# Kernel optimization log

Hardware: AMD Instinct MI355X
Metric: run time of the kernel (lower is better)

The kernel has to match this reference:

```python
import jax, jax.numpy as jnp
import numpy as np
from jax import lax

EMBED = 768
D_INNER = 2 * EMBED          # expand = 2
D_STATE = 16
D_CONV = 4
DT_RANK = (EMBED + 15) // 16  # 48
FF = 3072
B, L = 2, 1024


def setup_inputs() -> dict:
    key = jax.random.key(0)
    ks = jax.random.split(key, 20)
    s = 0.02
    inp = {
        "x": jax.random.normal(ks[0], (B, L, EMBED), jnp.float32),
        # Mamba params
        "in_proj_w": jax.random.normal(ks[1], (2 * D_INNER, EMBED), jnp.float32) * s,
        "conv_w": jax.random.normal(ks[2], (D_INNER, 1, D_CONV), jnp.float32) * s,
        "conv_b": jnp.zeros((D_INNER,), jnp.float32),
        "x_proj_w": jax.random.normal(ks[3], (DT_RANK + 2 * D_STATE, D_INNER), jnp.float32) * s,
        "dt_proj_w": jax.random.normal(ks[4], (D_INNER, DT_RANK), jnp.float32) * s,
        "dt_proj_b": jax.random.normal(ks[5], (D_INNER,), jnp.float32) * s,
        "A_log": jnp.log(jnp.broadcast_to(jnp.arange(1, D_STATE + 1, dtype=jnp.float32), (D_INNER, D_STATE))),
        "D_param": jnp.ones((D_INNER,), jnp.float32),
        "out_proj_w": jax.random.normal(ks[6], (EMBED, D_INNER), jnp.float32) * s,
        # block params
        "ln1_w": jnp.ones((EMBED,), jnp.float32), "ln1_b": jnp.zeros((EMBED,), jnp.float32),
        "ln2_w": jnp.ones((EMBED,), jnp.float32), "ln2_b": jnp.zeros((EMBED,), jnp.float32),
        "ffn_w1": jax.random.normal(ks[7], (FF, EMBED), jnp.float32) * s,
        "ffn_b1": jnp.zeros((FF,), jnp.float32),
        "ffn_w2": jax.random.normal(ks[8], (EMBED, FF), jnp.float32) * s,
        "ffn_b2": jnp.zeros((EMBED,), jnp.float32),
    }
    return inp


def _layernorm(x, w, b, eps=1e-5):
    mu = jnp.mean(x, -1, keepdims=True)
    var = jnp.mean((x - mu) ** 2, -1, keepdims=True)
    return (x - mu) * lax.rsqrt(var + eps) * w + b


def _mamba(x, in_proj_w, conv_w, conv_b, x_proj_w, dt_proj_w, dt_proj_b,
           A_log, D_param, out_proj_w):
    # x: [B, L, E]
    xz = jnp.einsum('ble,de->bld', x, in_proj_w)          # [B,L,2*Di]
    xin, z = jnp.split(xz, 2, axis=-1)                    # [B,L,Di] each
    # causal depthwise conv over time
    xc = lax.conv_general_dilated(
        xin.transpose(0, 2, 1), conv_w, window_strides=(1,),
        padding=[(D_CONV - 1, 0)], feature_group_count=D_INNER,
        dimension_numbers=('NCH', 'OIH', 'NCH'))
    xc = (xc + conv_b[None, :, None]).transpose(0, 2, 1)  # [B,L,Di]
    xc = jax.nn.silu(xc)
    # input-dependent SSM params
    x_dbl = jnp.einsum('bld,rd->blr', xc, x_proj_w)       # [B,L,dt_rank+2n]
    dt, Bm, Cm = jnp.split(x_dbl, [DT_RANK, DT_RANK + D_STATE], axis=-1)
    delta = jax.nn.softplus(jnp.einsum('blr,dr->bld', dt, dt_proj_w) + dt_proj_b)
    A = -jnp.exp(A_log)                                   # [Di, n]
    deltaA = jnp.exp(jnp.einsum('bld,dn->bldn', delta, A))
    deltaBu = jnp.einsum('bld,bln,bld->bldn', delta, Bm, xc)

    def step(h, xs):
        dA, dBu, Ct = xs                                  # [B,Di,n],[B,Di,n],[B,n]
        h = dA * h + dBu
        y = jnp.einsum('bdn,bn->bd', h, Ct)
        return h, y

    h0 = jnp.zeros((x.shape[0], D_INNER, D_STATE), x.dtype)
    _, ys = lax.scan(step, h0, (deltaA.transpose(1, 0, 2, 3),
                                deltaBu.transpose(1, 0, 2, 3),
                                Cm.transpose(1, 0, 2)))
    y = ys.transpose(1, 0, 2)                             # [B,L,Di]
    y = y + xc * D_param
    y = y * jax.nn.silu(z)
    return jnp.einsum('bld,ed->ble', y, out_proj_w)


def reference(x, in_proj_w, conv_w, conv_b, x_proj_w, dt_proj_w, dt_proj_b,
              A_log, D_param, out_proj_w, ln1_w, ln1_b, ln2_w, ln2_b,
              ffn_w1, ffn_b1, ffn_w2, ffn_b2):
    # dropout is identity in eval mode
    h = _mamba(x, in_proj_w, conv_w, conv_b, x_proj_w, dt_proj_w, dt_proj_b,
               A_log, D_param, out_proj_w)
    x1 = _layernorm(h + x, ln1_w, ln1_b)
    f = jnp.einsum('ble,fe->blf', x1, ffn_w1) + ffn_b1
    f = jax.nn.gelu(f)
    f = jnp.einsum('blf,ef->ble', f, ffn_w2) + ffn_b2
    return _layernorm(f + x1, ln2_w, ln2_b)
```

## Files before the change

kernel.cpp:

```cpp
#include <hip/hip_runtime.h>
#include <math.h>

#define EMBED 768
#define DI 1536
#define DSTATE 16
#define DCONV 4
#define DTRANK 48
#define FF 3072
#define BATCH 2
#define SEQ 1024
#define NROWS (BATCH*SEQ)
#define TCH 32
#define NCH (SEQ/TCH)
#define DBLK 64

typedef __bf16 bf16x8 __attribute__((ext_vector_type(8)));
typedef float f32x4 __attribute__((ext_vector_type(4)));
typedef unsigned int u32x4 __attribute__((ext_vector_type(4)));

static __device__ __forceinline__ unsigned short f2b(float f) {
    union { float f; unsigned u; } v; v.f = f;
    unsigned r = v.u + 0x7FFFu + ((v.u >> 16) & 1u);
    return (unsigned short)(r >> 16);
}
static __device__ __forceinline__ float b2f(unsigned short s) {
    union { unsigned u; float f; } v; v.u = ((unsigned)s) << 16;
    return v.f;
}

#define GLOAD_LDS16(g, l) __builtin_amdgcn_global_load_lds( \
    (const __attribute__((address_space(1))) void*)(g), \
    (__attribute__((address_space(3))) void*)(l), 16, 0, 0)

template<int EPI, int KSPLIT>
__global__ __launch_bounds__(256)
void gemm_sk(const unsigned short* __restrict__ A,
             const unsigned short* __restrict__ W,
             float* __restrict__ C, unsigned short* __restrict__ Cb,
             float* __restrict__ part,
             int M, int N, int K,
             const float* __restrict__ bias)
{
    __shared__ alignas(16) unsigned short As[2][128 * 32];
    __shared__ alignas(16) unsigned short Ws[2][64 * 32];
    const int tid  = threadIdx.x;
    const int lane = tid & 63, wave = tid >> 6;
    const int bm = blockIdx.y * 128, bn = blockIdx.x * 64;
    const int kc = K / KSPLIT;
    const int kz = blockIdx.z * kc;
    const int ln = lane & 15, lg = lane >> 4;

    f32x4 acc[2][4];
    #pragma unroll
    for (int i = 0; i < 2; ++i)
        #pragma unroll
        for (int j = 0; j < 4; ++j)
            acc[i][j] = (f32x4){0.f, 0.f, 0.f, 0.f};

    const int ra = tid >> 2, ca = tid & 3;
    const int cs = (ca * 8) ^ ((ra & 3) << 3);
    const unsigned short* gA0 = A + (size_t)(bm + ra) * K + kz + cs;
    const unsigned short* gA1 = A + (size_t)(bm + ra + 64) * K + kz + cs;
    const unsigned short* gW  = W + (size_t)(bn + ra) * K + kz + cs;

#define STAGE(bf, kk) do { \
        GLOAD_LDS16(gA0 + (kk), &As[bf][wave * 512]); \
        GLOAD_LDS16(gA1 + (kk), &As[bf][2048 + wave * 512]); \
        GLOAD_LDS16(gW  + (kk), &Ws[bf][wave * 512]); \
    } while (0)

    STAGE(0, 0);
    __syncthreads();
    int buf = 0;
    for (int k0 = 0; k0 < kc; k0 += 32) {
        if (k0 + 32 < kc) STAGE(buf ^ 1, k0 + 32);
        bf16x8 af[2], wf[4];
        #pragma unroll
        for (int i = 0; i < 2; ++i) {
            int row = wave * 32 + i * 16 + ln;
            af[i] = *reinterpret_cast<const bf16x8*>(
                &As[buf][row * 32 + ((lg * 8) ^ ((row & 3) << 3))]);
        }
        #pragma unroll
        for (int j = 0; j < 4; ++j) {
            int row = j * 16 + ln;
            wf[j] = *reinterpret_cast<const bf16x8*>(
                &Ws[buf][row * 32 + ((lg * 8) ^ ((row & 3) << 3))]);
        }
        #pragma unroll
        for (int i = 0; i < 2; ++i)
            #pragma unroll
            for (int j = 0; j < 4; ++j)
                acc[i][j] = __builtin_amdgcn_mfma_f32_16x16x32_bf16(af[i], wf[j], acc[i][j], 0, 0, 0);
        __syncthreads();
        buf ^= 1;
    }
#undef STAGE

    if constexpr (KSPLIT > 1) {
        float* pb = part + (size_t)blockIdx.z * M * N;
        #pragma unroll
        for (int i = 0; i < 2; ++i)
            #pragma unroll
            for (int j = 0; j < 4; ++j) {
                int col = bn + j * 16 + ln;
                #pragma unroll
                for (int rr = 0; rr < 4; ++rr) {
                    int row = bm + wave * 32 + i * 16 + lg * 4 + rr;
                    pb[(size_t)row * N + col] = acc[i][j][rr];
                }
            }
    } else {
        #pragma unroll
        for (int i = 0; i < 2; ++i)
            #pragma unroll
            for (int j = 0; j < 4; ++j) {
                int col = bn + j * 16 + ln;
                #pragma unroll
                for (int rr = 0; rr < 4; ++rr) {
                    int row = bm + wave * 32 + i * 16 + lg * 4 + rr;
                    float v = acc[i][j][rr];
                    size_t o = (size_t)row * N + col;
                    if (EPI == 3) {
                        v += bias[col];
                        float t = 0.7978845608028654f * (v + 0.044715f * v * v * v);
                        Cb[o] = f2b(0.5f * v * (1.f + tanhf(t)));
                    } else if (EPI == 6) {
                        Cb[o] = f2b(v);
                    } else {
                        C[o] = v;
                    }
                }
            }
    }
}

template<int KS, int BIAS>
__global__ __launch_bounds__(256)
void reduce_ln(const float* __restrict__ part, const float* __restrict__ resid,
               const float* __restrict__ bias,
               const float* __restrict__ w, const float* __restrict__ bb,
               float* __restrict__ out, unsigned short* __restrict__ outb)
{
    const int row = blockIdx.x;
    const size_t ro = (size_t)row * EMBED;
    const int i0 = threadIdx.x, i1 = i0 + 256, i2 = i0 + 512;
    float v0 = 0.f, v1 = 0.f, v2 = 0.f;
    #pragma unroll
    for (int z = 0; z < KS; ++z) {
        const float* p = part + (size_t)z * NROWS * EMBED + ro;
        v0 += p[i0]; v1 += p[i1]; v2 += p[i2];
    }
    if (BIAS) { v0 += bias[i0]; v1 += bias[i1]; v2 += bias[i2]; }
    v0 += resid[ro + i0]; v1 += resid[ro + i1]; v2 += resid[ro + i2];

    float s  = v0 + v1 + v2;
    float s2 = v0 * v0 + v1 * v1 + v2 * v2;
    #pragma unroll
    for (int m = 1; m < 64; m <<= 1) {
        s  += __shfl_xor(s,  m);
        s2 += __shfl_xor(s2, m);
    }
    __shared__ float sh1[4], sh2[4];
    int wv = threadIdx.x >> 6;
    if ((threadIdx.x & 63) == 0) { sh1[wv] = s; sh2[wv] = s2; }
    __syncthreads();
    float S1 = sh1[0] + sh1[1] + sh1[2] + sh1[3];
    float S2 = sh2[0] + sh2[1] + sh2[2] + sh2[3];
    float mu  = S1 * (1.f / EMBED);
    float var = S2 * (1.f / EMBED) - mu * mu;
    float rs  = rsqrtf(var + 1e-5f);
    float o0 = (v0 - mu) * rs * w[i0] + bb[i0];
    float o1 = (v1 - mu) * rs * w[i1] + bb[i1];
    float o2 = (v2 - mu) * rs * w[i2] + bb[i2];
    out[ro + i0] = o0; out[ro + i1] = o1; out[ro + i2] = o2;
    if (outb) {
        outb[ro + i0] = f2b(o0); outb[ro + i1] = f2b(o1); outb[ro + i2] = f2b(o2);
    }
}

__global__ __launch_bounds__(256)
void xproj_mfma(const unsigned short* __restrict__ A,
                const unsigned short* __restrict__ W,
                float* __restrict__ part)
{
    const int mt = blockIdx.x, s = blockIdx.y;
    const int lane = threadIdx.x & 63, wave = threadIdx.x >> 6;
    const int ln = lane & 15, lg = lane >> 4;
    const int row0 = mt * 128 + wave * 32;
    const int kb = s * 192;
    f32x4 acc[2][5];
    #pragma unroll
    for (int i = 0; i < 2; ++i)
        #pragma unroll
        for (int j = 0; j < 5; ++j)
            acc[i][j] = (f32x4){0.f, 0.f, 0.f, 0.f};

    for (int kk = 0; kk < 192; kk += 32) {
        const int k = kb + kk + lg * 8;
        bf16x8 af[2], wf[5];
        af[0] = *reinterpret_cast<const bf16x8*>(A + (size_t)(row0 + ln) * DI + k);
        af[1] = *reinterpret_cast<const bf16x8*>(A + (size_t)(row0 + 16 + ln) * DI + k);
        #pragma unroll
        for (int j = 0; j < 5; ++j)
            wf[j] = *reinterpret_cast<const bf16x8*>(W + (size_t)(j * 16 + ln) * DI + k);
        #pragma unroll
        for (int i = 0; i < 2; ++i)
            #pragma unroll
            for (int j = 0; j < 5; ++j)
                acc[i][j] = __builtin_amdgcn_mfma_f32_16x16x32_bf16(af[i], wf[j], acc[i][j], 0, 0, 0);
    }
    float* pb = part + (size_t)s * NROWS * 80;
    #pragma unroll
    for (int i = 0; i < 2; ++i)
        #pragma unroll
        for (int j = 0; j < 5; ++j)
            #pragma unroll
            for (int rr = 0; rr < 4; ++rr) {
                int row = row0 + i * 16 + lg * 4 + rr;
                int col = j * 16 + ln;
                pb[(size_t)row * 80 + col] = acc[i][j][rr];
            }
}

__global__ __launch_bounds__(256)
void xproj_reduce(const float* __restrict__ part, float* __restrict__ xdbl,
                  unsigned short* __restrict__ xdblb)
{
    int idx = blockIdx.x * 256 + threadIdx.x;
    float sum = 0.f;
    #pragma unroll
    for (int s = 0; s < 8; ++s) sum += part[(size_t)s * NROWS * 80 + idx];
    xdbl[idx] = sum;
    int col = idx % 80, row = idx / 80;
    if (col < 48)      xdblb[row * 64 + col] = f2b(sum);
    else if (col < 64) xdblb[row * 64 + col] = 0;
}

__global__ __launch_bounds__(256)
void cvt7_k(const float* __restrict__ x,  const float* __restrict__ w1,
            const float* __restrict__ w2, const float* __restrict__ w3,
            const float* __restrict__ w4, const float* __restrict__ w5,
            const float* __restrict__ w6,
            unsigned short* __restrict__ xb,  unsigned short* __restrict__ w1b,
            unsigned short* __restrict__ w2b, unsigned short* __restrict__ w3b,
            unsigned short* __restrict__ w4b, unsigned short* __restrict__ w5b,
            unsigned short* __restrict__ w6b)
{
    size_t i4 = ((size_t)blockIdx.x * 256 + threadIdx.x) * 4;
    if (i4 >= 9953280u) {
        int off = (int)(i4 - 9953280u);
        if (off >= 98304) return;
        int row = off >> 6, colb = off & 63;
        ushort4 u = {0, 0, 0, 0};
        if (colb < 48) {
            float4 v = *reinterpret_cast<const float4*>(w6 + row * 48 + colb);
            u.x = f2b(v.x); u.y = f2b(v.y); u.z = f2b(v.z); u.w = f2b(v.w);
        }
        *reinterpret_cast<ushort4*>(w6b + off) = u;
        return;
    }
    const float* src; unsigned short* dst; size_t off;
    if      (i4 < 1572864u) { src = x;  dst = xb;  off = i4; }
    else if (i4 < 3932160u) { src = w1; dst = w1b; off = i4 - 1572864u; }
    else if (i4 < 5111808u) { src = w2; dst = w2b; off = i4 - 3932160u; }
    else if (i4 < 7471104u) { src = w3; dst = w3b; off = i4 - 5111808u; }
    else if (i4 < 9830400u) { src = w4; dst = w4b; off = i4 - 7471104u; }
    else                    { src = w5; dst = w5b; off = i4 - 9830400u; }
    float4 v = *reinterpret_cast<const float4*>(src + off);
    ushort4 u;
    u.x = f2b(v.x); u.y = f2b(v.y); u.z = f2b(v.z); u.w = f2b(v.w);
    *reinterpret_cast<ushort4*>(dst + off) = u;
}

__global__ __launch_bounds__(256)
void conv_silu_k(const unsigned short* __restrict__ xz, const float* __restrict__ cw,
                 const float* __restrict__ cb, unsigned short* __restrict__ xcb)
{
    int q = blockIdx.x * 256 + threadIdx.x;
    int d4 = (q * 4) % DI;
    int bt = (q * 4) / DI;
    int t  = bt % SEQ;
    const unsigned short* base = xz + (size_t)bt * (2 * DI) + d4;
    float4 acc = *reinterpret_cast<const float4*>(cb + d4);
    float4 wv0 = *reinterpret_cast<const float4*>(cw + (d4 + 0) * 4);
    float4 wv1 = *reinterpret_cast<const float4*>(cw + (d4 + 1) * 4);
    float4 wv2 = *reinterpret_cast<const float4*>(cw + (d4 + 2) * 4);
    float4 wv3 = *reinterpret_cast<const float4*>(cw + (d4 + 3) * 4);
    {
        ushort4 r = *reinterpret_cast<const ushort4*>(base);
        acc.x += wv0.w * b2f(r.x); acc.y += wv1.w * b2f(r.y);
        acc.z += wv2.w * b2f(r.z); acc.w += wv3.w * b2f(r.w);
    }
    if (t >= 1) {
        ushort4 r = *reinterpret_cast<const ushort4*>(base - 2 * DI);
        acc.x += wv0.z * b2f(r.x); acc.y += wv1.z * b2f(r.y);
        acc.z += wv2.z * b2f(r.z); acc.w += wv3.z * b2f(r.w);
    }
    if (t >= 2) {
        ushort4 r = *reinterpret_cast<const ushort4*>(base - 4 * DI);
        acc.x += wv0.y * b2f(r.x); acc.y += wv1.y * b2f(r.y);
        acc.z += wv2.y * b2f(r.z); acc.w += wv3.y * b2f(r.w);
    }
    if (t >= 3) {
        ushort4 r = *reinterpret_cast<const ushort4*>(base - 6 * DI);
        acc.x += wv0.x * b2f(r.x); acc.y += wv1.x * b2f(r.y);
        acc.z += wv2.x * b2f(r.z); acc.w += wv3.x * b2f(r.w);
    }
    ushort4 u;
    u.x = f2b(acc.x / (1.f + __expf(-acc.x)));
    u.y = f2b(acc.y / (1.f + __expf(-acc.y)));
    u.z = f2b(acc.z / (1.f + __expf(-acc.z)));
    u.w = f2b(acc.w / (1.f + __expf(-acc.w)));
    *reinterpret_cast<ushort4*>(xcb + (size_t)bt * DI + d4) = u;
}

static __device__ __forceinline__ void dt_mfma(
    const unsigned short (*xd_s)[72], float (*del_s)[DBLK + 4],
    const unsigned short* __restrict__ wdtb, const float* __restrict__ dtb,
    int d0, int wave, int ln, int lg)
{
    f32x4 dacc[2];
    dacc[0] = (f32x4){0.f, 0.f, 0.f, 0.f};
    dacc[1] = (f32x4){0.f, 0.f, 0.f, 0.f};
    const unsigned short* wrow = wdtb + (size_t)(d0 + wave * 16 + ln) * 64;
    #pragma unroll
    for (int kk = 0; kk < 2; ++kk) {
        bf16x8 wf = *reinterpret_cast<const bf16x8*>(wrow + kk * 32 + lg * 8);
        #pragma unroll
        for (int i = 0; i < 2; ++i) {
            bf16x8 a = *reinterpret_cast<const bf16x8*>(&xd_s[i * 16 + ln][kk * 32 + lg * 8]);
            dacc[i] = __builtin_amdgcn_mfma_f32_16x16x32_bf16(a, wf, dacc[i], 0, 0, 0);
        }
    }
    float bias_d = dtb[d0 + wave * 16 + ln];
    #pragma unroll
    for (int i = 0; i < 2; ++i)
        #pragma unroll
        for (int rr = 0; rr < 4; ++rr) {
            float v = dacc[i][rr] + bias_d;
            del_s[i * 16 + lg * 4 + rr][wave * 16 + ln] =
                (v > 20.f) ? v : log1pf(__expf(v));
        }
}

__global__ __launch_bounds__(256)
void scan2_a(const unsigned short* __restrict__ xdblb, const unsigned short* __restrict__ wdtb,
             const float* __restrict__ dtb,  const unsigned short* __restrict__ xcb,
             const float* __restrict__ xdbl, const float* __restrict__ A_log,
             float* __restrict__ hfin, float* __restrict__ aprod)
{
    const int d0 = blockIdx.x * DBLK, ch = blockIdx.y, b = blockIdx.z;
    const int t0 = ch * TCH;
    __shared__ float del_s[TCH][DBLK + 4];
    __shared__ unsigned short xd_s[TCH][72];
    __shared__ unsigned short xc_s[TCH][DBLK + 8];
    __shared__ float b_s[TCH][20];
    const int tid = threadIdx.x;
    {
        const int cz = tid & 7, tz = tid >> 3;
        size_t rz = (size_t)(b * SEQ + t0 + tz);
        *reinterpret_cast<u32x4*>(&xc_s[tz][cz * 8]) =
            *reinterpret_cast<const u32x4*>(&xcb[rz * DI + d0 + cz * 8]);
        *reinterpret_cast<u32x4*>(&xd_s[tz][cz * 8]) =
            *reinterpret_cast<const u32x4*>(&xdblb[rz * 64 + cz * 8]);
        const int cbq = tid & 3, tb = tid >> 2;
        if (tb < TCH) {
            size_t rowo = (size_t)(b * SEQ + t0 + tb);
            *reinterpret_cast<float4*>(&b_s[tb][cbq * 4]) =
                *reinterpret_cast<const float4*>(&xdbl[rowo * 80 + DTRANK + cbq * 4]);
        }
    }
    __syncthreads();
    const int lane = tid & 63, wave = tid >> 6;
    const int ln = lane & 15, lg = lane >> 4;
    dt_mfma(xd_s, del_s, wdtb, dtb, d0, wave, ln, lg);
    __syncthreads();

    const int wd = wave * 16 + (lane >> 2);
    const int d = d0 + wd;
    const int nq = (lane & 3) * 4;
    float4 Av = *reinterpret_cast<const float4*>(&A_log[d * DSTATE + nq]);
    const float A0 = -__expf(Av.x), A1 = -__expf(Av.y), A2 = -__expf(Av.z), A3 = -__expf(Av.w);
    float h0_ = 0.f, h1_ = 0.f, h2_ = 0.f, h3_ = 0.f;
    float p0 = 1.f, p1 = 1.f, p2 = 1.f, p3 = 1.f;
    #pragma unroll 4
    for (int t = 0; t < TCH; ++t) {
        float dl = del_s[t][wd];
        float u  = dl * b2f(xc_s[t][wd]);
        float4 bq = *reinterpret_cast<const float4*>(&b_s[t][nq]);
        float e0 = __expf(dl * A0), e1 = __expf(dl * A1);
        float e2 = __expf(dl * A2), e3 = __expf(dl * A3);
        h0_ = e0 * h0_ + u * bq.x; p0 *= e0;
        h1_ = e1 * h1_ + u * bq.y; p1 *= e1;
        h2_ = e2 * h2_ + u * bq.z; p2 *= e2;
        h3_ = e3 * h3_ + u * bq.w; p3 *= e3;
    }
    size_t o = ((size_t)((b * NCH + ch) * DI) + d) * DSTATE + nq;
    *reinterpret_cast<float4*>(&hfin[o])  = (float4){h0_, h1_, h2_, h3_};
    *reinterpret_cast<float4*>(&aprod[o]) = (float4){p0, p1, p2, p3};
}

__global__ __launch_bounds__(256)
void scan2_c(const unsigned short* __restrict__ xdblb, const unsigned short* __restrict__ wdtb,
             const float* __restrict__ dtb,  const unsigned short* __restrict__ xcb,
             const float* __restrict__ xdbl, const float* __restrict__ A_log,
             const float* __restrict__ Dp,   const unsigned short* __restrict__ xz,
             const float* __restrict__ hfin, const float* __restrict__ aprod,
             unsigned short* __restrict__ yb)
{
    const int d0 = blockIdx.x * DBLK, ch = blockIdx.y, b = blockIdx.z;
    const int t0 = ch * TCH;
    __shared__ float del_s[TCH][DBLK + 4];
    __shared__ unsigned short xd_s[TCH][72];
    __shared__ unsigned short xc_s[TCH][DBLK + 8];
    __shared__ float b_s[TCH][20];
    __shared__ float c_s[TCH][20];
    __shared__ unsigned short z_s[TCH][DBLK + 8];
    const int tid = threadIdx.x;
    {
        const int cz = tid & 7, tz = tid >> 3;
        size_t rz = (size_t)(b * SEQ + t0 + tz);
        *reinterpret_cast<u32x4*>(&xc_s[tz][cz * 8]) =
            *reinterpret_cast<const u32x4*>(&xcb[rz * DI + d0 + cz * 8]);
        *reinterpret_cast<u32x4*>(&z_s[tz][cz * 8]) =
            *reinterpret_cast<const u32x4*>(&xz[rz * (2 * DI) + DI + d0 + cz * 8]);
        *reinterpret_cast<u32x4*>(&xd_s[tz][cz * 8]) =
            *reinterpret_cast<const u32x4*>(&xdblb[rz * 64 + cz * 8]);
        const int cbq = tid & 3, tb = tid >> 2;
        if (tb < TCH) {
            size_t rowo = (size_t)(b * SEQ + t0 + tb);
            *reinterpret_cast<float4*>(&b_s[tb][cbq * 4]) =
                *reinterpret_cast<const float4*>(&xdbl[rowo * 80 + DTRANK + cbq * 4]);
        } else {
            size_t rowo = (size_t)(b * SEQ + t0 + tb - TCH);
            *reinterpret_cast<float4*>(&c_s[tb - TCH][cbq * 4]) =
                *reinterpret_cast<const float4*>(&xdbl[rowo * 80 + DTRANK + DSTATE + cbq * 4]);
        }
    }
    const int lane = tid & 63, wave = tid >> 6;
    const int ln = lane & 15, lg = lane >> 4;
    const int wd = wave * 16 + (lane >> 2);
    const int d = d0 + wd;
    const int nq = (lane & 3) * 4;

    float4 h = {0.f, 0.f, 0.f, 0.f};
    for (int cc = 0; cc < ch; ++cc) {
        size_t o = ((size_t)((b * NCH + cc) * DI) + d) * DSTATE + nq;
        float4 a = *reinterpret_cast<const float4*>(&aprod[o]);
        float4 f = *reinterpret_cast<const float4*>(&hfin[o]);
        h.x = a.x * h.x + f.x; h.y = a.y * h.y + f.y;
        h.z = a.z * h.z + f.z; h.w = a.w * h.w + f.w;
    }

    __syncthreads();
    dt_mfma(xd_s, del_s, wdtb, dtb, d0, wave, ln, lg);
    __syncthreads();

    float4 Av = *reinterpret_cast<const float4*>(&A_log[d * DSTATE + nq]);
    const float A0 = -__expf(Av.x), A1 = -__expf(Av.y), A2 = -__expf(Av.z), A3 = -__expf(Av.w);
    const float Dd = Dp[d];
    unsigned short* yrow = yb + (size_t)(b * SEQ + t0) * DI + d;
    #pragma unroll 4
    for (int t = 0; t < TCH; ++t) {
        float dl = del_s[t][wd];
        float xv = b2f(xc_s[t][wd]);
        float u  = dl * xv;
        float4 bq = *reinterpret_cast<const float4*>(&b_s[t][nq]);
        float4 cq = *reinterpret_cast<const float4*>(&c_s[t][nq]);
        float e0 = __expf(dl * A0), e1 = __expf(dl * A1);
        float e2 = __expf(dl * A2), e3 = __expf(dl * A3);
        h.x = e0 * h.x + u * bq.x;
        h.y = e1 * h.y + u * bq.y;
        h.z = e2 * h.z + u * bq.z;
        h.w = e3 * h.w + u * bq.w;
        float py = h.x * cq.x + h.y * cq.y + h.z * cq.z + h.w * cq.w;
        py += __shfl_xor(py, 1);
        py += __shfl_xor(py, 2);
        if ((lane & 3) == 0) {
            float yv = py + xv * Dd;
            float zv = b2f(z_s[t][wd]);
            yv *= zv / (1.f + __expf(-zv));
            yrow[(size_t)t * DI] = f2b(yv);
        }
    }
}

extern "C" void kernel_launch(void* const* d_in, const int* in_sizes, int n_in,
                              void* d_out, int out_size, void* d_ws, size_t ws_size,
                              hipStream_t stream)
{
    const float* x         = (const float*)d_in[0];
    const float* in_proj_w = (const float*)d_in[1];
    const float* conv_w    = (const float*)d_in[2];
    const float* conv_b    = (const float*)d_in[3];
    const float* x_proj_w  = (const float*)d_in[4];
    const float* dt_proj_w = (const float*)d_in[5];
    const float* dt_proj_b = (const float*)d_in[6];
    const float* A_log     = (const float*)d_in[7];
    const float* D_param   = (const float*)d_in[8];
    const float* out_proj_w= (const float*)d_in[9];
    const float* ln1_w     = (const float*)d_in[10];
    const float* ln1_b     = (const float*)d_in[11];
    const float* ln2_w     = (const float*)d_in[12];
    const float* ln2_b     = (const float*)d_in[13];
    const float* ffn_w1    = (const float*)d_in[14];
    const float* ffn_b1    = (const float*)d_in[15];
    const float* ffn_w2    = (const float*)d_in[16];
    const float* ffn_b2    = (const float*)d_in[17];
    float* out = (float*)d_out;

    char* Wp = (char*)d_ws;
    #define MB(n) ((size_t)(n) * 1048576)
    unsigned short* xzb   = (unsigned short*)(Wp + 0);
    unsigned short* xcb   = (unsigned short*)(Wp + MB(16));
    float*          xdbl  = (float*)         (Wp + MB(24));
    unsigned short* xdblb = (unsigned short*)(Wp + MB(26));
    unsigned short* ybb   = (unsigned short*)(Wp + MB(28));
    float*          hfin  = (float*)         (Wp + MB(36));
    float*          aprod = (float*)         (Wp + MB(44));
    unsigned short* xb    = (unsigned short*)(Wp + MB(52));
    unsigned short* wib   = (unsigned short*)(Wp + MB(56));
    unsigned short* wob   = (unsigned short*)(Wp + MB(61));
    unsigned short* wf1b  = (unsigned short*)(Wp + MB(64));
    unsigned short* wf2b  = (unsigned short*)(Wp + MB(69));
    unsigned short* xpwb  = (unsigned short*)(Wp + MB(74));
    unsigned short* wdtb  = (unsigned short*)(Wp + MB(75));
    float*          part  = (float*)         (Wp + MB(76));
    float*          part_op = (float*)       (Wp + MB(82));
    float*          part_f2 = (float*)       (Wp + MB(108));
    float*          x1    = (float*)         (Wp + MB(134));
    unsigned short* x1b   = (unsigned short*)(Wp + MB(141));
    unsigned short* fbf   = (unsigned short*)(Wp + MB(145));
    #undef MB

    dim3 blk(256);

    cvt7_k<<<9816, blk, 0, stream>>>(x, in_proj_w, out_proj_w, ffn_w1, ffn_w2, x_proj_w,
                                     dt_proj_w, xb, wib, wob, wf1b, wf2b, xpwb, wdtb);

    gemm_sk<6, 1><<<dim3(48, 16, 1), blk, 0, stream>>>(xb, wib, nullptr, xzb, nullptr,
                                                       NROWS, 2 * DI, EMBED, nullptr);

    conv_silu_k<<<(BATCH * SEQ * DI) / 1024, blk, 0, stream>>>(xzb, conv_w, conv_b, xcb);

    xproj_mfma<<<dim3(16, 8), blk, 0, stream>>>(xcb, xpwb, part);
    xproj_reduce<<<640, blk, 0, stream>>>(part, xdbl, xdblb);

    scan2_a<<<dim3(DI / DBLK, NCH, BATCH), blk, 0, stream>>>(
        xdblb, wdtb, dt_proj_b, xcb, xdbl, A_log, hfin, aprod);
    scan2_c<<<dim3(DI / DBLK, NCH, BATCH), blk, 0, stream>>>(
        xdblb, wdtb, dt_proj_b, xcb, xdbl, A_log, D_param, xzb, hfin, aprod, ybb);

    gemm_sk<0, 4><<<dim3(12, 16, 4), blk, 0, stream>>>(ybb, wob, nullptr, nullptr, part_op,
                                                       NROWS, EMBED, DI, nullptr);
    reduce_ln<4, 0><<<NROWS, blk, 0, stream>>>(part_op, x, nullptr, ln1_w, ln1_b, x1, x1b);

    gemm_sk<3, 1><<<dim3(48, 16, 1), blk, 0, stream>>>(x1b, wf1b, nullptr, fbf, nullptr,
                                                       NROWS, FF, EMBED, ffn_b1);

    gemm_sk<0, 4><<<dim3(12, 16, 4), blk, 0, stream>>>(fbf, wf2b, nullptr, nullptr, part_f2,
                                                       NROWS, EMBED, FF, nullptr);
    reduce_ln<4, 1><<<NROWS, blk, 0, stream>>>(part_f2, x1, ffn_b2, ln2_w, ln2_b, out, nullptr);
}
```

Measured before the change: 203.6 us.

## Fuse chunked two-pass selective scan into single sequential per-channel scan kernel

Replaces the two-kernel chunked scan (per-chunk state/decay products, then prefix and output) with one kernel where each 64-thread block scans all chunks sequentially for 16 channels. It keeps the state in registers and prefetches the next chunk's inputs into registers. This removes the intermediate hfin/aprod buffers and one launch, but cuts the grid to 192 single-wave blocks and serializes 1024 timesteps per block, sharply reducing parallelism.

```diff
diff --git a/kernel.cpp b/kernel.cpp
--- a/kernel.cpp
+++ b/kernel.cpp
@@ -12,7 +12,6 @@
 #define NROWS (BATCH*SEQ)
 #define TCH 32
 #define NCH (SEQ/TCH)
-#define DBLK 64
 
 typedef __bf16 bf16x8 __attribute__((ext_vector_type(8)));
 typedef float f32x4 __attribute__((ext_vector_type(4)));
@@ -315,175 +314,119 @@
     *reinterpret_cast<ushort4*>(xcb + (size_t)bt * DI + d4) = u;
 }
 
-static __device__ __forceinline__ void dt_mfma(
-    const unsigned short (*xd_s)[72], float (*del_s)[DBLK + 4],
-    const unsigned short* __restrict__ wdtb, const float* __restrict__ dtb,
-    int d0, int wave, int ln, int lg)
-{
-    f32x4 dacc[2];
-    dacc[0] = (f32x4){0.f, 0.f, 0.f, 0.f};
-    dacc[1] = (f32x4){0.f, 0.f, 0.f, 0.f};
-    const unsigned short* wrow = wdtb + (size_t)(d0 + wave * 16 + ln) * 64;
-    #pragma unroll
-    for (int kk = 0; kk < 2; ++kk) {
-        bf16x8 wf = *reinterpret_cast<const bf16x8*>(wrow + kk * 32 + lg * 8);
-        #pragma unroll
-        for (int i = 0; i < 2; ++i) {
-            bf16x8 a = *reinterpret_cast<const bf16x8*>(&xd_s[i * 16 + ln][kk * 32 + lg * 8]);
-            dacc[i] = __builtin_amdgcn_mfma_f32_16x16x32_bf16(a, wf, dacc[i], 0, 0, 0);
-        }
-    }
-    float bias_d = dtb[d0 + wave * 16 + ln];
-    #pragma unroll
-    for (int i = 0; i < 2; ++i)
-        #pragma unroll
-        for (int rr = 0; rr < 4; ++rr) {
-            float v = dacc[i][rr] + bias_d;
-            del_s[i * 16 + lg * 4 + rr][wave * 16 + ln] =
-                (v > 20.f) ? v : log1pf(__expf(v));
-        }
-}
-
-__global__ __launch_bounds__(256)
-void scan2_a(const unsigned short* __restrict__ xdblb, const unsigned short* __restrict__ wdtb,
-             const float* __restrict__ dtb,  const unsigned short* __restrict__ xcb,
-             const float* __restrict__ xdbl, const float* __restrict__ A_log,
-             float* __restrict__ hfin, float* __restrict__ aprod)
-{
-    const int d0 = blockIdx.x * DBLK, ch = blockIdx.y, b = blockIdx.z;
-    const int t0 = ch * TCH;
-    __shared__ float del_s[TCH][DBLK + 4];
+__global__ __launch_bounds__(64)
+void scan3(const unsigned short* __restrict__ xdblb, const unsigned short* __restrict__ wdtb,
+           const float* __restrict__ dtb,  const unsigned short* __restrict__ xcb,
+           const float* __restrict__ xdbl, const float* __restrict__ A_log,
+           const float* __restrict__ Dp,   const unsigned short* __restrict__ xz,
+           unsigned short* __restrict__ yb)
+{
+    const int d0 = blockIdx.x * 16, b = blockIdx.y;
+    __shared__ float del_s[TCH][20];
     __shared__ unsigned short xd_s[TCH][72];
-    __shared__ unsigned short xc_s[TCH][DBLK + 8];
-    __shared__ float b_s[TCH][20];
-    const int tid = threadIdx.x;
-    {
-        const int cz = tid & 7, tz = tid >> 3;
-        size_t rz = (size_t)(b * SEQ + t0 + tz);
-        *reinterpret_cast<u32x4*>(&xc_s[tz][cz * 8]) =
-            *reinterpret_cast<const u32x4*>(&xcb[rz * DI + d0 + cz * 8]);
-        *reinterpret_cast<u32x4*>(&xd_s[tz][cz * 8]) =
-            *reinterpret_cast<const u32x4*>(&xdblb[rz * 64 + cz * 8]);
-        const int cbq = tid & 3, tb = tid >> 2;
-        if (tb < TCH) {
-            size_t rowo = (size_t)(b * SEQ + t0 + tb);
-            *reinterpret_cast<float4*>(&b_s[tb][cbq * 4]) =
-                *reinterpret_cast<const float4*>(&xdbl[rowo * 80 + DTRANK + cbq * 4]);
-        }
-    }
-    __syncthreads();
-    const int lane = tid & 63, wave = tid >> 6;
-    const int ln = lane & 15, lg = lane >> 4;
-    dt_mfma(xd_s, del_s, wdtb, dtb, d0, wave, ln, lg);
-    __syncthreads();
-
-    const int wd = wave * 16 + (lane >> 2);
-    const int d = d0 + wd;
-    const int nq = (lane & 3) * 4;
-    float4 Av = *reinterpret_cast<const float4*>(&A_log[d * DSTATE + nq]);
-    const float A0 = -__expf(Av.x), A1 = -__expf(Av.y), A2 = -__expf(Av.z), A3 = -__expf(Av.w);
-    float h0_ = 0.f, h1_ = 0.f, h2_ = 0.f, h3_ = 0.f;
-    float p0 = 1.f, p1 = 1.f, p2 = 1.f, p3 = 1.f;
-    #pragma unroll 4
-    for (int t = 0; t < TCH; ++t) {
-        float dl = del_s[t][wd];
-        float u  = dl * b2f(xc_s[t][wd]);
-        float4 bq = *reinterpret_cast<const float4*>(&b_s[t][nq]);
-        float e0 = __expf(dl * A0), e1 = __expf(dl * A1);
-        float e2 = __expf(dl * A2), e3 = __expf(dl * A3);
-        h0_ = e0 * h0_ + u * bq.x; p0 *= e0;
-        h1_ = e1 * h1_ + u * bq.y; p1 *= e1;
-        h2_ = e2 * h2_ + u * bq.z; p2 *= e2;
-        h3_ = e3 * h3_ + u * bq.w; p3 *= e3;
-    }
-    size_t o = ((size_t)((b * NCH + ch) * DI) + d) * DSTATE + nq;
-    *reinterpret_cast<float4*>(&hfin[o])  = (float4){h0_, h1_, h2_, h3_};
-    *reinterpret_cast<float4*>(&aprod[o]) = (float4){p0, p1, p2, p3};
-}
-
-__global__ __launch_bounds__(256)
-void scan2_c(const unsigned short* __restrict__ xdblb, const unsigned short* __restrict__ wdtb,
-             const float* __restrict__ dtb,  const unsigned short* __restrict__ xcb,
-             const float* __restrict__ xdbl, const float* __restrict__ A_log,
-             const float* __restrict__ Dp,   const unsigned short* __restrict__ xz,
-             const float* __restrict__ hfin, const float* __restrict__ aprod,
-             unsigned short* __restrict__ yb)
-{
-    const int d0 = blockIdx.x * DBLK, ch = blockIdx.y, b = blockIdx.z;
-    const int t0 = ch * TCH;
-    __shared__ float del_s[TCH][DBLK + 4];
-    __shared__ unsigned short xd_s[TCH][72];
-    __shared__ unsigned short xc_s[TCH][DBLK + 8];
+    __shared__ unsigned short xc_s[TCH][24];
+    __shared__ unsigned short z_s[TCH][24];
     __shared__ float b_s[TCH][20];
     __shared__ float c_s[TCH][20];
-    __shared__ unsigned short z_s[TCH][DBLK + 8];
-    const int tid = threadIdx.x;
-    {
-        const int cz = tid & 7, tz = tid >> 3;
-        size_t rz = (size_t)(b * SEQ + t0 + tz);
-        *reinterpret_cast<u32x4*>(&xc_s[tz][cz * 8]) =
-            *reinterpret_cast<const u32x4*>(&xcb[rz * DI + d0 + cz * 8]);
-        *reinterpret_cast<u32x4*>(&z_s[tz][cz * 8]) =
-            *reinterpret_cast<const u32x4*>(&xz[rz * (2 * DI) + DI + d0 + cz * 8]);
-        *reinterpret_cast<u32x4*>(&xd_s[tz][cz * 8]) =
-            *reinterpret_cast<const u32x4*>(&xdblb[rz * 64 + cz * 8]);
-        const int cbq = tid & 3, tb = tid >> 2;
-        if (tb < TCH) {
-            size_t rowo = (size_t)(b * SEQ + t0 + tb);
-            *reinterpret_cast<float4*>(&b_s[tb][cbq * 4]) =
-                *reinterpret_cast<const float4*>(&xdbl[rowo * 80 + DTRANK + cbq * 4]);
-        } else {
-            size_t rowo = (size_t)(b * SEQ + t0 + tb - TCH);
-            *reinterpret_cast<float4*>(&c_s[tb - TCH][cbq * 4]) =
-                *reinterpret_cast<const float4*>(&xdbl[rowo * 80 + DTRANK + DSTATE + cbq * 4]);
-        }
-    }
-    const int lane = tid & 63, wave = tid >> 6;
+
+    const int lane = threadIdx.x;
     const int ln = lane & 15, lg = lane >> 4;
-    const int wd = wave * 16 + (lane >> 2);
+    const int wd = lane >> 2;
+    const int nq = (lane & 3) * 4;
     const int d = d0 + wd;
-    const int nq = (lane & 3) * 4;
-
-    float4 h = {0.f, 0.f, 0.f, 0.f};
-    for (int cc = 0; cc < ch; ++cc) {
-        size_t o = ((size_t)((b * NCH + cc) * DI) + d) * DSTATE + nq;
-        float4 a = *reinterpret_cast<const float4*>(&aprod[o]);
-        float4 f = *reinterpret_cast<const float4*>(&hfin[o]);
-        h.x = a.x * h.x + f.x; h.y = a.y * h.y + f.y;
-        h.z = a.z * h.z + f.z; h.w = a.w * h.w + f.w;
-    }
-
-    __syncthreads();
-    dt_mfma(xd_s, del_s, wdtb, dtb, d0, wave, ln, lg);
-    __syncthreads();
+    const int srow = lane >> 1, sh = lane & 1;
+
+    u32x4 rxd[4], rxc, rzv;
+    float4 rb[2], rc[2];
+
+#define LOAD_REGS(ch) do { \
+        size_t rr_ = (size_t)(b * SEQ + (ch) * TCH + srow); \
+        _Pragma("unroll") \
+        for (int j = 0; j < 4; ++j) \
+            rxd[j] = *reinterpret_cast<const u32x4*>(&xdblb[rr_ * 64 + (size_t)(sh * 4 + j) * 8]); \
+        rxc = *reinterpret_cast<const u32x4*>(&xcb[rr_ * DI + d0 + sh * 8]); \
+        rzv = *reinterpret_cast<const u32x4*>(&xz[rr_ * (2 * DI) + DI + d0 + sh * 8]); \
+        _Pragma("unroll") \
+        for (int j = 0; j < 2; ++j) { \
+            rb[j] = *reinterpret_cast<const float4*>(&xdbl[rr_ * 80 + 48 + (size_t)(sh * 2 + j) * 4]); \
+            rc[j] = *reinterpret_cast<const float4*>(&xdbl[rr_ * 80 + 64 + (size_t)(sh * 2 + j) * 4]); \
+        } \
+    } while (0)
+
+    LOAD_REGS(0);
 
     float4 Av = *reinterpret_cast<const float4*>(&A_log[d * DSTATE + nq]);
     const float A0 = -__expf(Av.x), A1 = -__expf(Av.y), A2 = -__expf(Av.z), A3 = -__expf(Av.w);
     const float Dd = Dp[d];
-    unsigned short* yrow = yb + (size_t)(b * SEQ + t0) * DI + d;
-    #pragma unroll 4
-    for (int t = 0; t < TCH; ++t) {
-        float dl = del_s[t][wd];
-        float xv = b2f(xc_s[t][wd]);
-        float u  = dl * xv;
-        float4 bq = *reinterpret_cast<const float4*>(&b_s[t][nq]);
-        float4 cq = *reinterpret_cast<const float4*>(&c_s[t][nq]);
-        float e0 = __expf(dl * A0), e1 = __expf(dl * A1);
-        float e2 = __expf(dl * A2), e3 = __expf(dl * A3);
-        h.x = e0 * h.x + u * bq.x;
-        h.y = e1 * h.y + u * bq.y;
-        h.z = e2 * h.z + u * bq.z;
-        h.w = e3 * h.w + u * bq.w;
-        float py = h.x * cq.x + h.y * cq.y + h.z * cq.z + h.w * cq.w;
-        py += __shfl_xor(py, 1);
-        py += __shfl_xor(py, 2);
-        if ((lane & 3) == 0) {
-            float yv = py + xv * Dd;
-            float zv = b2f(z_s[t][wd]);
-            yv *= zv / (1.f + __expf(-zv));
-            yrow[(size_t)t * DI] = f2b(yv);
+    const float bias_d = dtb[d0 + ln];
+    const unsigned short* wrow = wdtb + (size_t)(d0 + ln) * 64;
+
+    float4 h = {0.f, 0.f, 0.f, 0.f};
+
+    for (int ch = 0; ch < NCH; ++ch) {
+        __syncthreads();
+        #pragma unroll
+        for (int j = 0; j < 4; ++j)
+            *reinterpret_cast<u32x4*>(&xd_s[srow][(sh * 4 + j) * 8]) = rxd[j];
+        *reinterpret_cast<u32x4*>(&xc_s[srow][sh * 8]) = rxc;
+        *reinterpret_cast<u32x4*>(&z_s[srow][sh * 8]) = rzv;
+        #pragma unroll
+        for (int j = 0; j < 2; ++j) {
+            *reinterpret_cast<float4*>(&b_s[srow][(sh * 2 + j) * 4]) = rb[j];
+            *reinterpret_cast<float4*>(&c_s[srow][(sh * 2 + j) * 4]) = rc[j];
         }
-    }
+        __syncthreads();
+        if (ch + 1 < NCH) LOAD_REGS(ch + 1);
+
+        {
+            f32x4 dacc[2];
+            dacc[0] = (f32x4){0.f, 0.f, 0.f, 0.f};
+            dacc[1] = (f32x4){0.f, 0.f, 0.f, 0.f};
+            #pragma unroll
+            for (int kk = 0; kk < 2; ++kk) {
+                bf16x8 wf = *reinterpret_cast<const bf16x8*>(wrow + kk * 32 + lg * 8);
+                #pragma unroll
+                for (int i = 0; i < 2; ++i) {
+                    bf16x8 a = *reinterpret_cast<const bf16x8*>(&xd_s[i * 16 + ln][kk * 32 + lg * 8]);
+                    dacc[i] = __builtin_amdgcn_mfma_f32_16x16x32_bf16(a, wf, dacc[i], 0, 0, 0);
+                }
+            }
+            #pragma unroll
+            for (int i = 0; i < 2; ++i)
+                #pragma unroll
+                for (int rr = 0; rr < 4; ++rr) {
+                    float v = dacc[i][rr] + bias_d;
+                    del_s[i * 16 + lg * 4 + rr][ln] = (v > 20.f) ? v : log1pf(__expf(v));
+                }
+        }
+        __syncthreads();
+
+        unsigned short* yrow = yb + (size_t)(b * SEQ + ch * TCH) * DI + d;
+        #pragma unroll 4
+        for (int t = 0; t < TCH; ++t) {
+            float dl = del_s[t][wd];
+            float xv = b2f(xc_s[t][wd]);
+            float u  = dl * xv;
+            float4 bq = *reinterpret_cast<const float4*>(&b_s[t][nq]);
+            float4 cq = *reinterpret_cast<const float4*>(&c_s[t][nq]);
+            float e0 = __expf(dl * A0), e1 = __expf(dl * A1);
+            float e2 = __expf(dl * A2), e3 = __expf(dl * A3);
+            h.x = e0 * h.x + u * bq.x;
+            h.y = e1 * h.y + u * bq.y;
+            h.z = e2 * h.z + u * bq.z;
+            h.w = e3 * h.w + u * bq.w;
+            float py = h.x * cq.x + h.y * cq.y + h.z * cq.z + h.w * cq.w;
+            py += __shfl_xor(py, 1);
+            py += __shfl_xor(py, 2);
+            if ((lane & 3) == 0) {
+                float yv = py + xv * Dd;
+                float zv = b2f(z_s[t][wd]);
+                yv *= zv / (1.f + __expf(-zv));
+                yrow[(size_t)t * DI] = f2b(yv);
+            }
+        }
+    }
+#undef LOAD_REGS
 }
 
 extern "C" void kernel_launch(void* const* d_in, const int* in_sizes, int n_in,
@@ -517,21 +460,19 @@
     float*          xdbl  = (float*)         (Wp + MB(24));
     unsigned short* xdblb = (unsigned short*)(Wp + MB(26));
     unsigned short* ybb   = (unsigned short*)(Wp + MB(28));
-    float*          hfin  = (float*)         (Wp + MB(36));
-    float*          aprod = (float*)         (Wp + MB(44));
-    unsigned short* xb    = (unsigned short*)(Wp + MB(52));
-    unsigned short* wib   = (unsigned short*)(Wp + MB(56));
-    unsigned short* wob   = (unsigned short*)(Wp + MB(61));
-    unsigned short* wf1b  = (unsigned short*)(Wp + MB(64));
-    unsigned short* wf2b  = (unsigned short*)(Wp + MB(69));
-    unsigned short* xpwb  = (unsigned short*)(Wp + MB(74));
-    unsigned short* wdtb  = (unsigned short*)(Wp + MB(75));
-    float*          part  = (float*)         (Wp + MB(76));
-    float*          part_op = (float*)       (Wp + MB(82));
-    float*          part_f2 = (float*)       (Wp + MB(108));
-    float*          x1    = (float*)         (Wp + MB(134));
-    unsigned short* x1b   = (unsigned short*)(Wp + MB(141));
-    unsigned short* fbf   = (unsigned short*)(Wp + MB(145));
+    unsigned short* xb    = (unsigned short*)(Wp + MB(36));
+    unsigned short* wib   = (unsigned short*)(Wp + MB(40));
+    unsigned short* wob   = (unsigned short*)(Wp + MB(45));
+    unsigned short* wf1b  = (unsigned short*)(Wp + MB(48));
+    unsigned short* wf2b  = (unsigned short*)(Wp + MB(53));
+    unsigned short* xpwb  = (unsigned short*)(Wp + MB(58));
+    unsigned short* wdtb  = (unsigned short*)(Wp + MB(59));
+    float*          part  = (float*)         (Wp + MB(60));
+    float*          part_op = (float*)       (Wp + MB(66));
+    float*          part_f2 = (float*)       (Wp + MB(92));
+    float*          x1    = (float*)         (Wp + MB(118));
+    unsigned short* x1b   = (unsigned short*)(Wp + MB(125));
+    unsigned short* fbf   = (unsigned short*)(Wp + MB(129));
     #undef MB
 
     dim3 blk(256);
@@ -547,10 +488,8 @@
     xproj_mfma<<<dim3(16, 8), blk, 0, stream>>>(xcb, xpwb, part);
     xproj_reduce<<<640, blk, 0, stream>>>(part, xdbl, xdblb);
 
-    scan2_a<<<dim3(DI / DBLK, NCH, BATCH), blk, 0, stream>>>(
-        xdblb, wdtb, dt_proj_b, xcb, xdbl, A_log, hfin, aprod);
-    scan2_c<<<dim3(DI / DBLK, NCH, BATCH), blk, 0, stream>>>(
-        xdblb, wdtb, dt_proj_b, xcb, xdbl, A_log, D_param, xzb, hfin, aprod, ybb);
+    scan3<<<dim3(DI / 16, BATCH), dim3(64), 0, stream>>>(
+        xdblb, wdtb, dt_proj_b, xcb, xdbl, A_log, D_param, xzb, ybb);
 
     gemm_sk<0, 4><<<dim3(12, 16, 4), blk, 0, stream>>>(ybb, wob, nullptr, nullptr, part_op,
                                                        NROWS, EMBED, DI, nullptr);
```

New measurement: 431.7 us. 2.12x slower.
